# Kernel tuning notes

Hardware: AMD Instinct MI355X
Metric: run time of the kernel (lower is better)

Reference implementation:

```python
import jax, jax.numpy as jnp
import numpy as np
from jax import lax

N = 2048


def setup_inputs() -> dict:
    key = jax.random.key(0)
    k1, k2, k3, k4 = jax.random.split(key, 4)
    root_logits = jax.random.normal(k1, (N,), jnp.float32)
    e = jax.random.normal(k2, (N, N), jnp.float32)
    # torch init zeros the diagonal of edge_probs
    edge_logits = e * (1.0 - jnp.eye(N, dtype=jnp.float32))
    # Gumbel noise made explicit so the reference is deterministic
    g_root = jax.random.gumbel(k3, (2, N), jnp.float32)
    g_edge = jax.random.gumbel(k4, (N, 2, N), jnp.float32)
    return {"root_logits": root_logits, "edge_logits": edge_logits,
            "g_root": g_root, "g_edge": g_edge}


def _sample_dag(root_logits, edge_logits, g_root, g_edge):
    n = root_logits.shape[0]
    f32 = jnp.float32
    i32 = jnp.int32

    # --- root sampling: hard gumbel-softmax over {root, not-root}, tau=1 ---
    yr = jnp.stack([jax.nn.log_sigmoid(root_logits),
                    jax.nn.log_sigmoid(-root_logits)]) + g_root  # [2, n]
    soft_r = jax.nn.softmax(yr, axis=0)[0]
    root_bool = yr[0] > yr[1]
    # straight-through: hard forward, soft gradient
    roots = root_bool.astype(f32) + soft_r - lax.stop_gradient(soft_r)

    # --- per-node edge sampling (noise pre-drawn; rows masked by BFS) ---
    ye = jnp.stack([jax.nn.log_sigmoid(edge_logits),
                    jax.nn.log_sigmoid(-edge_logits)], axis=1) + g_edge  # [n,2,n]
    soft_e = jax.nn.softmax(ye, axis=1)[:, 0, :]  # [n, n]
    hard_e = ye[:, 0, :] > ye[:, 1, :]            # [n, n] bool
    st_e = hard_e.astype(f32) + soft_e - lax.stop_gradient(soft_e)

    # --- FIFO queue init with roots in ascending index order ---
    idx = jnp.arange(n, dtype=i32)
    rank = jnp.cumsum(root_bool.astype(i32)) - 1
    pos = jnp.where(root_bool, rank, n)  # slot n is a write-only dump
    queue0 = jnp.zeros(n + 1, i32).at[pos].set(idx, mode='drop')
    tail0 = jnp.sum(root_bool).astype(i32)
    head0 = jnp.int32(0)
    dag0 = jnp.zeros((n, n), f32)
    anc0 = jnp.eye(n, dtype=bool)  # ancestors, anc[i,i]=1
    enq0 = root_bool               # dedup flag (equivalent to torch's pop-skip)

    def step(carry, _):
        dag, anc, queue, enq, head, tail = carry
        active = head < tail
        i = queue[head]
        anc_i = anc[i]  # includes i itself (eye init)
        cand = (1.0 - anc_i.astype(f32)) * (1.0 - roots)
        row = st_e[i] * cand
        dag = dag.at[i].set(jnp.where(active, row, dag[i]))
        children = hard_e[i] & (~anc_i) & (~root_bool) & active
        # anc[j] |= anc[i] | {i} for each child j (anc_i already contains i)
        anc = anc | (children[:, None] & anc_i[None, :])
        new = children & (~enq)
        r = jnp.cumsum(new.astype(i32)) - 1
        p = jnp.where(new, tail + r, n)
        queue = queue.at[p].set(idx, mode='drop')
        enq = enq | new
        tail = tail + jnp.sum(new).astype(i32)
        head = head + active.astype(i32)
        return (dag, anc, queue, enq, head, tail), None

    (dag, _, _, _, _, _), _ = lax.scan(
        step, (dag0, anc0, queue0, enq0, head0, tail0), None, length=n)
    return dag


def reference(root_logits, edge_logits, g_root, g_edge):
    return _sample_dag(root_logits, edge_logits, g_root, g_edge)
```

## Files before the change

### kernel.cpp

```cpp
#include <hip/hip_runtime.h>
#include <stdint.h>

typedef unsigned long long u64;
typedef unsigned int u32;
typedef unsigned short u16;

#define NN 2048
#define NW 32

#if __has_builtin(__builtin_amdgcn_sbfe)
#define SBFE(x, o) ((u32)__builtin_amdgcn_sbfe((int)(x), (u32)(o), 1u))
#else
#define SBFE(x, o) ((u32)(-(int)(((x) >> (o)) & 1u)))
#endif

static __device__ __forceinline__ bool gumbel_gt(float x, float g0, float g1) {
    float L = log1pf(expf(-fabsf(x)));
    float a = (-(fmaxf(-x, 0.f) + L)) + g0;
    float b = (-(fmaxf( x, 0.f) + L)) + g1;
    return a > b;
}

static __device__ __forceinline__ u64 orsel2(u64 acc, u64 w0, u64 w1, u64 m, int b0) {
    u32 mm = (b0 < 32) ? (u32)m : (u32)(m >> 32);
    int sh = b0 & 31;
    u32 s0 = SBFE(mm, sh);
    u32 s1 = SBFE(mm, sh + 1);
    u32 al = (u32)acc | ((u32)w0 & s0) | ((u32)w1 & s1);
    u32 ah = (u32)(acc >> 32) | ((u32)(w0 >> 32) & s0) | ((u32)(w1 >> 32) & s1);
    return ((u64)ah << 32) | al;
}

__global__ __launch_bounds__(256) void prep_kernel(
    const float* __restrict__ edge_logits,
    const float* __restrict__ g_edge,
    u64* __restrict__ heBits)
{
    const int i = blockIdx.x;
    const int t = threadIdx.x;
    const int lane = t & 63;
    const int wave = t >> 6;
    for (int c = wave; c < NW; c += 4) {
        int j = (c << 6) + lane;
        float x  = edge_logits[(size_t)i * NN + j];
        float g0 = g_edge[(size_t)i * (2 * NN) + j];
        float g1 = g_edge[(size_t)i * (2 * NN) + NN + j];
        u64 m = __ballot(gumbel_gt(x, g0, g1));
        if (lane == 0) heBits[(size_t)i * NW + c] = m;
    }
}

static __device__ void order_body(char* smem,
    const float* __restrict__ root_logits, const float* __restrict__ g_root,
    const u64* __restrict__ heBits,
    u16* __restrict__ posr, u16* __restrict__ porderW, int* __restrict__ nrPtr)
{
    int* s_porder = (int*)smem;
    int* s_cnt    = (int*)(smem + 8192);
    u64 (*s_U)[NW]  = (u64(*)[NW])(smem + 16384);
    u64 (*s_Pg)[NW] = (u64(*)[NW])(smem + 20480);
    u16* s_pos = (u16*)(smem + 24576);
    u16* s_f   = (u16*)(smem + 28672);
    u16* s_rk  = (u16*)(smem + 32768);
    u64* s_root = (u64*)(smem + 36864);
    u64* s_enq  = (u64*)(smem + 37120);
    u64* s_F    = (u64*)(smem + 37376);
    int* s_wsum = (int*)(smem + 37632);
    int* s_woff = (int*)(smem + 37696);
    int* s_sc   = (int*)(smem + 37760);
    int &s_base = s_sc[0]; int &s_lo = s_sc[1]; int &s_levcnt = s_sc[2];
    int &s_newcnt = s_sc[3]; int &s_nr = s_sc[4];

    const int t    = threadIdx.x;
    const int lane = t & 63;
    const int wid  = t >> 6;
    const int half = lane >> 5;
    const int w    = lane & 31;

    for (int p = 0; p < 2; ++p) {
        int j = p * 1024 + t;
        bool rb = gumbel_gt(root_logits[j], g_root[j], g_root[NN + j]);
        u64 m = __ballot(rb);
        if (lane == 0) s_root[j >> 6] = m;
    }
    __syncthreads();
    for (int p = 0; p < 2; ++p) {
        int j = p * 1024 + t;
        int ww = j >> 6; u64 bit = 1ull << (j & 63);
        if (s_root[ww] & bit) {
            int r = 0;
            for (int k = 0; k < ww; ++k) r += __popcll(s_root[k]);
            r += __popcll(s_root[ww] & (bit - 1ull));
            s_pos[j] = (u16)r;
            s_porder[r] = j;
        }
    }
    if (t < NW) s_enq[t] = s_root[t];
    if (t == 0) {
        int tl = 0;
        for (int k = 0; k < NW; ++k) tl += __popcll(s_root[k]);
        s_lo = 0; s_levcnt = tl; s_base = tl; s_nr = tl;
    }
    __syncthreads();

    while (s_levcnt > 0 && s_base < NN) {
        const int lo = s_lo, cnt = s_levcnt, base = s_base;
        const int seglen = (cnt + 15) >> 4;
        const int s0 = wid * seglen;
        const int s1 = (s0 + seglen < cnt) ? (s0 + seglen) : cnt;

        {
            u64 acc = 0;
            for (int m = s0 + half; m < s1; m += 2)
                acc |= heBits[(size_t)s_porder[lo + m] * NW + w];
            acc |= __shfl(acc, lane ^ 32);
            if (half == 0) s_U[wid][w] = acc;
        }
        __syncthreads();
        if (t < NW) {
            u64 o = 0;
            #pragma unroll
            for (int s = 0; s < 16; ++s) o |= s_U[s][t];
            s_F[t] = o & ~s_enq[t] & ~s_root[t];
        }
        __syncthreads();
        if (t < 512) {
            int s = t >> 5, ww = t & 31;
            u64 p = 0;
            for (int s2 = 0; s2 < s; ++s2) p |= s_U[s2][ww];
            s_Pg[s][ww] = p & s_F[ww];
        }
        __syncthreads();
        {
            u64 P  = s_Pg[wid][w];
            u64 Fw = s_F[w];
            int myidx = (s0 + lane < s1) ? s_porder[lo + s0 + lane] : 0;
            u64 rnext = 0;
            {
                int rowi0 = __shfl(myidx, half);
                if (s0 + half < s1) rnext = heBits[(size_t)rowi0 * NW + w];
            }
            for (int m = s0; m < s1; m += 2) {
                int m0 = m + half;
                u64 r = rnext;
                {
                    int sidx = (m + 2 - s0) + half;
                    if (sidx > 63) sidx = 0;
                    int rowin = __shfl(myidx, sidx);
                    rnext = 0;
                    if (m + 2 + half < s1) rnext = heBits[(size_t)rowin * NW + w];
                }
                u64 v = (m0 < s1) ? (r & Fw & ~P) : 0ull;
                u64 vlo = __shfl(v, w);
                u64 B = half ? (v & ~vlo) : v;
                int pc = __popcll(B);
                int inc = pc;
                #pragma unroll
                for (int d = 1; d < 32; d <<= 1) {
                    int u2 = __shfl_up(inc, d, 64);
                    if (w >= d) inc += u2;
                }
                int excl = inc - pc;
                int tot = __shfl(inc, (half << 5) | 31);
                if (w == 0 && m0 < s1) s_cnt[m0] = tot;
                u64 mm = B;
                int idx = excl;
                while (mm) {
                    int b = __ffsll(mm) - 1; mm &= mm - 1;
                    int j = (w << 6) + b;
                    s_f[j]  = (u16)m0;
                    s_rk[j] = (u16)idx++;
                }
                P |= B | __shfl(B, lane ^ 32);
            }
        }
        __syncthreads();
        {
            int b0 = 2 * t, b1 = 2 * t + 1;
            int c0 = (b0 < cnt) ? s_cnt[b0] : 0;
            int c1 = (b1 < cnt) ? s_cnt[b1] : 0;
            int pairv = c0 + c1;
            int incl = pairv;
            for (int d = 1; d < 64; d <<= 1) {
                int v = __shfl_up(incl, d, 64);
                if (lane >= d) incl += v;
            }
            if (lane == 63) s_wsum[wid] = incl;
            __syncthreads();
            if (t < 16) {
                int v = s_wsum[t];
                int inc2 = v;
                for (int d = 1; d < 16; d <<= 1) {
                    int u = __shfl_up(inc2, d, 16);
                    if (t >= d) inc2 += u;
                }
                s_woff[t] = inc2 - v;
                if (t == 15) s_newcnt = inc2;
            }
            __syncthreads();
            int excl = s_woff[wid] + (incl - pairv);
            if (b0 < cnt) s_cnt[b0] = excl;
            if (b1 < cnt) s_cnt[b1] = excl + c0;
        }
        __syncthreads();
        for (int p = 0; p < 2; ++p) {
            int j = p * 1024 + t;
            int ww = j >> 6;
            if ((s_F[ww] >> (j & 63)) & 1ull) {
                int slot = base + s_cnt[s_f[j]] + s_rk[j];
                s_pos[j] = (u16)slot;
                s_porder[slot] = j;
            }
        }
        if (t < NW) s_enq[t] |= s_F[t];
        __syncthreads();
        if (t == 0) { s_lo = base; s_levcnt = s_newcnt; s_base = base + s_newcnt; }
        __syncthreads();
    }

    for (int p = 0; p < 2; ++p) {
        int j = p * 1024 + t;
        int ww = j >> 6; u64 bit = 1ull << (j & 63);
        if (!((s_enq[ww] >> (j & 63)) & 1ull)) {
            int rk = 0;
            for (int k2 = 0; k2 < ww; ++k2) rk += __popcll(~s_enq[k2]);
            rk += __popcll(~s_enq[ww] & (bit - 1ull));
            int slot = s_base + rk;
            s_pos[j] = (u16)slot;
            s_porder[slot] = j;
        }
    }
    __syncthreads();
    for (int p = 0; p < 2; ++p) {
        int j = p * 1024 + t;
        int fl = s_pos[j];
        if ((s_root[j >> 6] >> (j & 63)) & 1ull) fl |= 0x8000;
        if ((s_enq[j >> 6]  >> (j & 63)) & 1ull) fl |= 0x4000;
        posr[j] = (u16)fl;
        porderW[j] = (u16)s_porder[j];
    }
    if (t == 0) *nrPtr = s_nr;
}

__global__ __launch_bounds__(1024) void ordtrans_kernel(
    const float* __restrict__ root_logits,
    const float* __restrict__ g_root,
    const u64* __restrict__ heBits,
    u64* __restrict__ heT,
    u16* __restrict__ posr,
    u16* __restrict__ porderW,
    int* __restrict__ nrPtr)
{
    __shared__ __align__(16) char smem[38016];
    const int bid  = blockIdx.x;
    const int t    = threadIdx.x;
    const int lane = t & 63;
    const int wv   = t >> 6;

    if (bid == 0) {
        order_body(smem, root_logits, g_root, heBits, posr, porderW, nrPtr);
    } else {
        int gw = (bid - 1) * 16 + wv;
        if (gw < 1024) {
            int ti = gw >> 5, tj = gw & 31;
            u64 w = heBits[(size_t)(64 * ti + lane) * NW + tj];
            u64 out = 0;
            #pragma unroll
            for (int b = 0; b < 64; ++b) {
                u64 m = __ballot(((w >> b) & 1ull) != 0);
                if (b == lane) out = m;
            }
            heT[(size_t)(64 * tj + lane) * NW + ti] = out;
        }
    }
}

__global__ __launch_bounds__(256) void apbuild_kernel(
    const u64* __restrict__ heT, const u16* __restrict__ porderW,
    const int* __restrict__ nrPtr, u64* __restrict__ Ap)
{
    __shared__ u64 s_row[NW];
    __shared__ u16 s_inv[NN];
    __shared__ int s_invb, s_nr;
    const int b = blockIdx.x;
    const int t = threadIdx.x;
    for (int q = t; q < NN; q += 256) s_inv[q] = porderW[q];
    if (t == 0) { s_invb = porderW[b]; s_nr = *nrPtr; }
    __syncthreads();
    if (t < NW) s_row[t] = heT[(size_t)s_invb * NW + t];
    __syncthreads();
    const bool bge = (b >= s_nr);
    for (int pass = 0; pass < 8; ++pass) {
        int a = pass * 256 + t;
        int ia = s_inv[a];
        bool bit = bge && (a < b) &&
                   (((s_row[ia >> 6] >> (ia & 63)) & 1ull) != 0);
        u64 m = __ballot(bit);
        if ((t & 63) == 0) Ap[(size_t)b * NW + (a >> 6)] = m;
    }
}

__global__ __launch_bounds__(64) void diagap2_kernel(
    u64* __restrict__ Ap, u64* __restrict__ Di)
{
    const int i = blockIdx.x;
    const int j = blockIdx.y;
    if (j > i) return;
    __shared__ u64 sm[64];
    const int r = threadIdx.x;
    u64 M = Ap[(size_t)(64 * i + r) * NW + i] | (1ull << r);
    for (int s = 0; s < 6; ++s) {
        sm[r] = M;
        __syncthreads();
        u64 acc = 0;
        #pragma unroll
        for (int b = 0; b < 64; ++b)
            acc |= sm[b] & (0ull - ((M >> b) & 1ull));
        __syncthreads();
        M = acc;
    }
    if (j == i) { Di[64 * i + r] = M; return; }
    sm[r] = Ap[(size_t)(64 * i + r) * NW + j];
    __syncthreads();
    u64 acc = 0;
    #pragma unroll
    for (int b = 0; b < 64; ++b)
        acc |= sm[b] & (0ull - ((M >> b) & 1ull));
    Ap[(size_t)(64 * i + r) * NW + j] = acc;
}

__global__ __launch_bounds__(1024) void colhalf_kernel(
    const u64* __restrict__ Ap, const u64* __restrict__ Di,
    u64* __restrict__ Anc)
{
    __shared__ __align__(16) u64 colA[16][64];
    __shared__ u64 part[16][64];
    const int t  = threadIdx.x;
    const int r  = t & 63;
    const int wv = t >> 6;
    const int k    = blockIdx.x & 15;
    const int hb   = blockIdx.x >> 4;
    const int base = hb << 4;
    const int bend = base + 16;
    const int kk   = base + k;

    for (int row = t; row < 64 * kk; row += 1024)
        Anc[(size_t)row * NW + kk] = 0ull;

    if (t < 64) {
        u64 d = Di[64 * kk + r];
        colA[0][r] = d;
        Anc[(size_t)(64 * kk + r) * NW + kk] = d;
    }
    __syncthreads();

    const int j0 = kk + wv;

    for (int ib = kk + 1; ib < bend; ib += 4) {
        u64 m0[4], acc[4];
        #pragma unroll
        for (int g = 0; g < 4; ++g) {
            int ig = ib + g;
            bool v = (ig < bend);
            m0[g] = (v && (j0 < ib)) ? Ap[(size_t)(64 * ig + r) * NW + j0] : 0ull;
            acc[g] = 0ull;
        }
        u64 tm[3][3];
        #pragma unroll
        for (int s = 0; s < 3; ++s) {
            #pragma unroll
            for (int q = 0; q < 3; ++q) {
                int g = s + 1 + q;
                tm[s][q] = (g < 4 && (ib + g) < bend)
                    ? Ap[(size_t)(64 * (ib + g) + r) * NW + (ib + s)] : 0ull;
            }
        }

        if (j0 < ib) {
            const ulonglong2* rp = (const ulonglong2*)&colA[j0 - kk][0];
            #pragma unroll
            for (int bp = 0; bp < 32; ++bp) {
                ulonglong2 ww = rp[bp];
                #pragma unroll
                for (int g = 0; g < 4; ++g)
                    acc[g] = orsel2(acc[g], ww.x, ww.y, m0[g], 2 * bp);
            }
        }

        #pragma unroll
        for (int s = 0; s < 4; ++s) {
            const int i = ib + s;
            if (i < bend) {
                part[wv][r] = acc[s];
                __syncthreads();
                if (wv < 2) {
                    u64 red = part[0][r];
                    #pragma unroll
                    for (int p = 1; p < 16; ++p) red |= part[p][r];
                    if (wv == 0) colA[i - kk][r] = red;
                    else Anc[(size_t)(64 * i + r) * NW + kk] = red;
                }
                __syncthreads();
                if (s < 3 && (i + 1) < bend) {
                    const u64* rowp = colA[i - kk];
                    #pragma unroll
                    for (int bi = 0; bi < 4; ++bi) {
                        int b = 4 * wv + bi;
                        u64 w = rowp[b];
                        u32 wl = (u32)w, wh = (u32)(w >> 32);
                        #pragma unroll
                        for (int q = 0; q < 3; ++q) {
                            int g = s + 1 + q;
                            if (g < 4) {
                                u32 sm2 = (u32)(0u - (u32)((tm[s][q] >> b) & 1ull));
                                u32 al = (u32)acc[g] | (wl & sm2);
                                u32 ah = (u32)(acc[g] >> 32) | (wh & sm2);
                                acc[g] = ((u64)ah << 32) | al;
                            }
                        }
                    }
                }
            }
        }
    }
}

__global__ __launch_bounds__(256) void merge1_kernel(
    const u64* __restrict__ Bstar,
    const u64* __restrict__ CpRows,
    u64* __restrict__ Yp)
{
    __shared__ u64 SQ[256][17];
    __shared__ u64 PL[8][4];
    const int t    = threadIdx.x;
    const int lane = t & 63;
    const int wv   = t >> 6;
    const int grp  = lane >> 4;
    const int w    = lane & 15;
    const int rb   = blockIdx.x;
    const int q    = blockIdx.y;

    if (t < 32)
        PL[t >> 2][t & 3] = Bstar[(size_t)(8 * rb + (t >> 2)) * NW + 16 + 4 * q + (t & 3)];
    for (int s = t; s < 4096; s += 256)
        SQ[s >> 4][s & 15] = CpRows[(size_t)(256 * q + (s >> 4)) * NW + (s & 15)];
    __syncthreads();

    u64 acc0 = 0, acc1 = 0;
    #pragma unroll
    for (int cw = 0; cw < 4; ++cw) {
        u64 m0 = PL[2 * wv + 0][cw];
        u64 m1 = PL[2 * wv + 1][cw];
        #pragma unroll
        for (int cc = 0; cc < 16; ++cc) {
            u64 qq = SQ[cw * 64 + cc * 4 + grp][w];
            int sh = (cc & 7) * 4 + grp;
            u32 h0 = (cc < 8) ? (u32)m0 : (u32)(m0 >> 32);
            u32 h1 = (cc < 8) ? (u32)m1 : (u32)(m1 >> 32);
            u32 ql = (u32)qq, qh = (u32)(qq >> 32);
            u32 s;
            s = SBFE(h0, sh);
            acc0 = ((u64)(((u32)(acc0 >> 32)) | (qh & s)) << 32) | (((u32)acc0) | (ql & s));
            s = SBFE(h1, sh);
            acc1 = ((u64)(((u32)(acc1 >> 32)) | (qh & s)) << 32) | (((u32)acc1) | (ql & s));
        }
    }
    acc0 |= __shfl_xor(acc0, 16); acc0 |= __shfl_xor(acc0, 32);
    acc1 |= __shfl_xor(acc1, 16); acc1 |= __shfl_xor(acc1, 32);
    if (grp == 0) {
        size_t base = ((size_t)q * 1024 + 8 * rb + 2 * wv) * 16 + w;
        Yp[base] = acc0;
        Yp[base + 16] = acc1;
    }
}

__global__ __launch_bounds__(256) void merge2_kernel(
    const u64* __restrict__ Yp,
    const u64* __restrict__ Astar,
    u64* __restrict__ Xp)
{
    __shared__ u64 SQ[256][17];
    __shared__ u64 PL[8][4];
    const int t    = threadIdx.x;
    const int lane = t & 63;
    const int wv   = t >> 6;
    const int grp  = lane >> 4;
    const int w    = lane & 15;
    const int rb   = blockIdx.x;
    const int q    = blockIdx.y;

    if (t < 32) {
        size_t idx = (size_t)(8 * rb + (t >> 2)) * 16 + 4 * q + (t & 3);
        PL[t >> 2][t & 3] = Yp[idx] | Yp[idx + 16384] | Yp[idx + 32768] | Yp[idx + 49152];
    }
    for (int s = t; s < 4096; s += 256)
        SQ[s >> 4][s & 15] = Astar[(size_t)(256 * q + (s >> 4)) * NW + (s & 15)];
    __syncthreads();

    u64 acc0 = 0, acc1 = 0;
    #pragma unroll
    for (int cw = 0; cw < 4; ++cw) {
        u64 m0 = PL[2 * wv + 0][cw];
        u64 m1 = PL[2 * wv + 1][cw];
        #pragma unroll
        for (int cc = 0; cc < 16; ++cc) {
            u64 qq = SQ[cw * 64 + cc * 4 + grp][w];
            int sh = (cc & 7) * 4 + grp;
            u32 h0 = (cc < 8) ? (u32)m0 : (u32)(m0 >> 32);
            u32 h1 = (cc < 8) ? (u32)m1 : (u32)(m1 >> 32);
            u32 ql = (u32)qq, qh = (u32)(qq >> 32);
            u32 s;
            s = SBFE(h0, sh);
            acc0 = ((u64)(((u32)(acc0 >> 32)) | (qh & s)) << 32) | (((u32)acc0) | (ql & s));
            s = SBFE(h1, sh);
            acc1 = ((u64)(((u32)(acc1 >> 32)) | (qh & s)) << 32) | (((u32)acc1) | (ql & s));
        }
    }
    acc0 |= __shfl_xor(acc0, 16); acc0 |= __shfl_xor(acc0, 32);
    acc1 |= __shfl_xor(acc1, 16); acc1 |= __shfl_xor(acc1, 32);
    if (grp == 0) {
        size_t base = ((size_t)q * 1024 + 8 * rb + 2 * wv) * 16 + w;
        Xp[base] = acc0;
        Xp[base + 16] = acc1;
    }
}

__global__ __launch_bounds__(256) void foldout_kernel(
    const u64* __restrict__ heBits,
    const u64* __restrict__ Anc,
    const u64* __restrict__ Xp,
    const u16* __restrict__ posr,
    float* __restrict__ dag)
{
    __shared__ u64 s_anc[NW];
    __shared__ u64 s_he[NW];
    __shared__ u16 s_pr[NN];
    const int i = blockIdx.x;
    const int t = threadIdx.x;

    ((int4*)s_pr)[t] = ((const int4*)posr)[t];
    __syncthreads();
    const int fl = s_pr[i];
    const int pi = fl & 0x7FF;
    if (t < NW) {
        u64 v;
        if (pi >= 1024 && t < 16) {
            size_t idx = (size_t)(pi - 1024) * 16 + t;
            v = Xp[idx] | Xp[idx + 16384] | Xp[idx + 32768] | Xp[idx + 49152];
        } else {
            v = Anc[(size_t)pi * NW + t];
        }
        s_anc[t] = v;
        s_he[t]  = heBits[(size_t)i * NW + t];
    }
    __syncthreads();
    const bool reach_i = (fl & 0x4000) != 0;
    const int j0 = t * 8;
    float o[8];
    #pragma unroll
    for (int e = 0; e < 8; ++e) {
        int j = j0 + e;
        int pr = s_pr[j];
        int a = pr & 0x7FF;
        bool he = ((s_he[j >> 6] >> (j & 63)) & 1ull) != 0;
        bool anc = ((s_anc[a >> 6] >> (a & 63)) & 1ull) != 0;
        o[e] = (reach_i && he && ((pr & 0x8000) == 0) && !anc) ? 1.f : 0.f;
    }
    float4* outp = (float4*)(dag + (size_t)i * NN + j0);
    outp[0] = make_float4(o[0], o[1], o[2], o[3]);
    outp[1] = make_float4(o[4], o[5], o[6], o[7]);
}

extern "C" void kernel_launch(void* const* d_in, const int* in_sizes, int n_in,
                              void* d_out, int out_size, void* d_ws, size_t ws_size,
                              hipStream_t stream) {
    const float* root_logits = (const float*)d_in[0];
    const float* edge_logits = (const float*)d_in[1];
    const float* g_root      = (const float*)d_in[2];
    const float* g_edge      = (const float*)d_in[3];
    float* dag = (float*)d_out;

    char* ws = (char*)d_ws;
    u64* heBits  = (u64*)(ws);
    u64* heT     = (u64*)(ws + (512 << 10));
    u64* Ap      = (u64*)(ws + (1 << 20));
    u64* Anc     = (u64*)(ws + (1 << 20) + (512 << 10));
    u64* Di      = (u64*)(ws + (2 << 20));
    u16* posr    = (u16*)(ws + (2 << 20) + (192 << 10));
    u16* porderW = (u16*)(ws + (2 << 20) + (196 << 10));
    int* nrPtr   = (int*)(ws + (2 << 20) + (200 << 10));
    u64* Yp      = (u64*)(ws + (3 << 20));
    u64* Xp      = (u64*)(ws + (3 << 20) + (512 << 10));

    prep_kernel    <<<NN, 256, 0, stream>>>(edge_logits, g_edge, heBits);
    ordtrans_kernel<<<256, 1024, 0, stream>>>(root_logits, g_root, heBits, heT,
                                              posr, porderW, nrPtr);
    apbuild_kernel <<<NN, 256, 0, stream>>>(heT, porderW, nrPtr, Ap);
    diagap2_kernel <<<dim3(NW, NW), 64, 0, stream>>>(Ap, Di);
    colhalf_kernel <<<NW, 1024, 0, stream>>>(Ap, Di, Anc);
    merge1_kernel  <<<dim3(128, 4), 256, 0, stream>>>(Anc + (size_t)1024 * NW,
                                                      Ap + (size_t)1024 * NW, Yp);
    merge2_kernel  <<<dim3(128, 4), 256, 0, stream>>>(Yp, Anc, Xp);
    foldout_kernel <<<NN, 256, 0, stream>>>(heBits, Anc, Xp, posr, dag);
}
```

Measured before the change: 127.4 us.

## Fuse Ap construction and diagonal closure into one block-per-tile kernel

Merges the per-row Ap build kernel and the diagonal-block transitive-closure kernel into one kernel with one 1024-thread block per 64-row tile. The tile is kept in shared memory, the closure uses wave shuffles, and Ap and Di are written back once. This removes a launch and a global round trip of Ap. Off-diagonal propagation is now limited to columns in the same 16-block half, which cuts work. The cost is far fewer blocks (32 instead of 2048) and a serial single-wave closure step.

Measured after the change: 149.4 us. 17.3% more time.

```diff
diff --git a/kernel.cpp b/kernel.cpp
--- a/kernel.cpp
+++ b/kernel.cpp
@@ -275,58 +275,72 @@
     }
 }
 
-__global__ __launch_bounds__(256) void apbuild_kernel(
+__global__ __launch_bounds__(1024) void apdiag_kernel(
     const u64* __restrict__ heT, const u16* __restrict__ porderW,
-    const int* __restrict__ nrPtr, u64* __restrict__ Ap)
-{
-    __shared__ u64 s_row[NW];
+    const int* __restrict__ nrPtr, u64* __restrict__ Ap, u64* __restrict__ Di)
+{
     __shared__ u16 s_inv[NN];
-    __shared__ int s_invb, s_nr;
-    const int b = blockIdx.x;
-    const int t = threadIdx.x;
-    for (int q = t; q < NN; q += 256) s_inv[q] = porderW[q];
-    if (t == 0) { s_invb = porderW[b]; s_nr = *nrPtr; }
-    __syncthreads();
-    if (t < NW) s_row[t] = heT[(size_t)s_invb * NW + t];
-    __syncthreads();
-    const bool bge = (b >= s_nr);
-    for (int pass = 0; pass < 8; ++pass) {
-        int a = pass * 256 + t;
-        int ia = s_inv[a];
-        bool bit = bge && (a < b) &&
-                   (((s_row[ia >> 6] >> (ia & 63)) & 1ull) != 0);
-        u64 m = __ballot(bit);
-        if ((t & 63) == 0) Ap[(size_t)b * NW + (a >> 6)] = m;
-    }
-}
-
-__global__ __launch_bounds__(64) void diagap2_kernel(
-    u64* __restrict__ Ap, u64* __restrict__ Di)
-{
-    const int i = blockIdx.x;
-    const int j = blockIdx.y;
-    if (j > i) return;
-    __shared__ u64 sm[64];
-    const int r = threadIdx.x;
-    u64 M = Ap[(size_t)(64 * i + r) * NW + i] | (1ull << r);
-    for (int s = 0; s < 6; ++s) {
-        sm[r] = M;
-        __syncthreads();
-        u64 acc = 0;
-        #pragma unroll
-        for (int b = 0; b < 64; ++b)
-            acc |= sm[b] & (0ull - ((M >> b) & 1ull));
-        __syncthreads();
-        M = acc;
-    }
-    if (j == i) { Di[64 * i + r] = M; return; }
-    sm[r] = Ap[(size_t)(64 * i + r) * NW + j];
-    __syncthreads();
-    u64 acc = 0;
-    #pragma unroll
-    for (int b = 0; b < 64; ++b)
-        acc |= sm[b] & (0ull - ((M >> b) & 1ull));
-    Ap[(size_t)(64 * i + r) * NW + j] = acc;
+    __shared__ u64 s_row[64][NW];
+    __shared__ u64 s_di[64];
+    __shared__ int s_nr;
+    const int I    = blockIdx.x;
+    const int t    = threadIdx.x;
+    const int lane = t & 63;
+    const int wv   = t >> 6;
+    const int halfbase = (I >> 4) << 4;
+
+    s_inv[t] = porderW[t];
+    s_inv[t + 1024] = porderW[t + 1024];
+    if (t == 0) s_nr = *nrPtr;
+    __syncthreads();
+    const int nr = s_nr;
+
+    for (int m = 0; m < 4; ++m) {
+        const int br = 16 * m + wv;
+        const int b  = 64 * I + br;
+        const bool bge = (b >= nr);
+        const int invb = s_inv[b];
+        u64 rw = (lane < 32) ? heT[(size_t)invb * NW + lane] : 0ull;
+        for (int k = 0; k < NW; ++k) {
+            int a = 64 * k + lane;
+            int ia = s_inv[a];
+            u64 wword = __shfl(rw, ia >> 6);
+            bool bit = bge && (a < b) && (((wword >> (ia & 63)) & 1ull) != 0);
+            u64 mm = __ballot(bit);
+            if (lane == 0) s_row[br][k] = mm;
+        }
+    }
+    __syncthreads();
+
+    if (t < 64) {
+        u64 M = s_row[t][I] | (1ull << t);
+        for (int s = 0; s < 6; ++s) {
+            u64 acc = 0;
+            for (int b = 0; b < 64; ++b)
+                acc |= __shfl(M, b) & (0ull - ((M >> b) & 1ull));
+            M = acc;
+        }
+        s_di[t] = M;
+        Di[64 * I + t] = M;
+    }
+    __syncthreads();
+
+    {
+        int j = halfbase + wv;
+        if (j < I) {
+            u64 d = s_di[lane];
+            u64 acc = 0;
+            for (int b = 0; b < 64; ++b)
+                acc |= s_row[b][j] & (0ull - ((d >> b) & 1ull));
+            s_row[lane][j] = acc;
+        }
+    }
+    __syncthreads();
+
+    for (int q = 0; q < 2; ++q) {
+        int idx = q * 1024 + t;
+        Ap[(size_t)(64 * I + (idx >> 5)) * NW + (idx & 31)] = s_row[idx >> 5][idx & 31];
+    }
 }
 
 __global__ __launch_bounds__(1024) void colhalf_kernel(
@@ -595,8 +609,7 @@
     prep_kernel    <<<NN, 256, 0, stream>>>(edge_logits, g_edge, heBits);
     ordtrans_kernel<<<256, 1024, 0, stream>>>(root_logits, g_root, heBits, heT,
                                               posr, porderW, nrPtr);
-    apbuild_kernel <<<NN, 256, 0, stream>>>(heT, porderW, nrPtr, Ap);
-    diagap2_kernel <<<dim3(NW, NW), 64, 0, stream>>>(Ap, Di);
+    apdiag_kernel  <<<NW, 1024, 0, stream>>>(heT, porderW, nrPtr, Ap, Di);
     colhalf_kernel <<<NW, 1024, 0, stream>>>(Ap, Di, Anc);
     merge1_kernel  <<<dim3(128, 4), 256, 0, stream>>>(Anc + (size_t)1024 * NW,
                                                       Ap + (size_t)1024 * NW, Yp);
```
